# Kernel tuning notes

Measured on AMD Instinct MI355X. Metric: run time of the kernel, lower is better.

Reference implementation:

```python
import jax, jax.numpy as jnp
import numpy as np

B, OUT, IN = 512, 1024, 1024


def setup_inputs() -> dict:
    key = jax.random.key(0)
    k1, k2 = jax.random.split(key)
    X = jax.random.normal(k1, (B, IN), dtype=jnp.float32)
    # xavier_uniform for W: bound = sqrt(6/(in+out))
    bound = float(np.sqrt(6.0 / (IN + OUT)))
    W = jax.random.uniform(k2, (OUT, IN), dtype=jnp.float32, minval=-bound, maxval=bound)
    factors = jnp.ones((OUT, 1), dtype=jnp.float32)
    return {"X": X, "W": W, "factors": factors}


def reference(X, W, factors):
    # tropical (max-plus) matmul with per-output-row scaling of X:
    # out[b,o] = max_i ( W[o,i] + X[b,i] * factors[o] )
    sum_var = W[None, :, :] + X[:, None, :] * factors[None, :, :]  # (B, OUT, IN)
    return jnp.max(sum_var, axis=-1)  # (B, OUT)
```

## Files before the change

### kernel.cpp

```cpp
#include <hip/hip_runtime.h>
#include <stdint.h>


#define BDIM 512
#define OUTDIM 1024
#define INDIM 1024
#define BM 64
#define BN 64
#define BK 32
#define SPLITK 4
#define KCHUNK (INDIM / SPLITK)

__device__ __forceinline__ unsigned enc_f32(float f) {
    unsigned u = __float_as_uint(f);
    return (u & 0x80000000u) ? ~u : (u | 0x80000000u);
}
__device__ __forceinline__ float dec_f32(unsigned k) {
    unsigned u = (k & 0x80000000u) ? (k & 0x7FFFFFFFu) : ~k;
    return __uint_as_float(u);
}

__global__ __launch_bounds__(256, 2)
void smp_main_kernel(const float* __restrict__ X, const float* __restrict__ W,
                     const float* __restrict__ F, unsigned* __restrict__ outk) {
    __shared__ float Xs[BK][BM + 4];
    __shared__ float Ws[BK][BN + 4];
    __shared__ float Os[BM][BN + 1];

    const int tid = threadIdx.x;
    const int tx = tid & 15;
    const int ty = tid >> 4;
    const int ob = blockIdx.x * BN;
    const int bb = blockIdx.y * BM;
    const int kbase = blockIdx.z * KCHUNK;

    float f[4];
#pragma unroll
    for (int n = 0; n < 4; ++n) f[n] = F[ob + 4 * ty + n];

    float acc[4][4];
#pragma unroll
    for (int m = 0; m < 4; ++m)
#pragma unroll
        for (int n = 0; n < 4; ++n) acc[m][n] = -INFINITY;

    for (int kt = 0; kt < KCHUNK; kt += BK) {
#pragma unroll
        for (int r = 0; r < 2; ++r) {
            const int l2 = tid + r * 256;
            const int row = l2 >> 3;
            const int c4 = (l2 & 7) * 4;
            const float4 xv = *reinterpret_cast<const float4*>(
                &X[(size_t)(bb + row) * INDIM + kbase + kt + c4]);
            const float4 wv = *reinterpret_cast<const float4*>(
                &W[(size_t)(ob + row) * INDIM + kbase + kt + c4]);
            Xs[c4 + 0][row] = xv.x; Xs[c4 + 1][row] = xv.y;
            Xs[c4 + 2][row] = xv.z; Xs[c4 + 3][row] = xv.w;
            Ws[c4 + 0][row] = wv.x; Ws[c4 + 1][row] = wv.y;
            Ws[c4 + 2][row] = wv.z; Ws[c4 + 3][row] = wv.w;
        }
        __syncthreads();

#pragma unroll
        for (int i = 0; i < BK; ++i) {
            const float4 xv = *reinterpret_cast<const float4*>(&Xs[i][4 * tx]);
            const float4 wv = *reinterpret_cast<const float4*>(&Ws[i][4 * ty]);
            const float x[4] = {xv.x, xv.y, xv.z, xv.w};
            const float w[4] = {wv.x, wv.y, wv.z, wv.w};
#pragma unroll
            for (int m = 0; m < 4; ++m)
#pragma unroll
                for (int n = 0; n < 4; ++n)
                    acc[m][n] = fmaxf(acc[m][n], fmaf(x[m], f[n], w[n]));
        }
        __syncthreads();
    }

#pragma unroll
    for (int m = 0; m < 4; ++m)
#pragma unroll
        for (int n = 0; n < 4; ++n)
            Os[4 * tx + m][4 * ty + n] = acc[m][n];
    __syncthreads();

#pragma unroll
    for (int c = 0; c < 16; ++c) {
        const int flat = c * 256 + tid;
        const int bl = flat >> 6;
        const int ol = flat & 63;
        const unsigned key = enc_f32(Os[bl][ol]);
        atomicMax(&outk[(size_t)(bb + bl) * OUTDIM + ob + ol], key);
    }
}

__global__ __launch_bounds__(256)
void smp_decode_kernel(unsigned* __restrict__ data) {
    const int idx = blockIdx.x * 256 + threadIdx.x;
    uint4 v = reinterpret_cast<uint4*>(data)[idx];
    float4 o;
    o.x = dec_f32(v.x); o.y = dec_f32(v.y); o.z = dec_f32(v.z); o.w = dec_f32(v.w);
    reinterpret_cast<float4*>(data)[idx] = o;
}

extern "C" void kernel_launch(void* const* d_in, const int* in_sizes, int n_in,
                              void* d_out, int out_size, void* d_ws, size_t ws_size,
                              hipStream_t stream) {
    const float* X = (const float*)d_in[0];
    const float* W = (const float*)d_in[1];
    const float* F = (const float*)d_in[2];
    unsigned* outk = (unsigned*)d_out;

    hipMemsetAsync(d_out, 0, (size_t)out_size * sizeof(float), stream);

    dim3 grid(OUTDIM / BN, BDIM / BM, SPLITK);
    smp_main_kernel<<<grid, 256, 0, stream>>>(X, W, F, outk);

    const int nvec = out_size / 4;
    smp_decode_kernel<<<nvec / 256, 256, 0, stream>>>(outk);
}
```

Before: 96.41 us.

## Use 128x128 register tiles with split-K slices and a max-reduce combine pass

Enlarges the block tile to 128x128 with 8x8 per-thread accumulators and a single 64-wide K chunk per block, stored in swizzled float4 shared memory so there are no transposing scalar stores. The atomicMax on order-preserving integer keys, the memset and the decode pass are replaced by plain writes of 16 partial slices to the workspace, followed by a combine kernel that takes their max. This raises the compute-to-shared-load ratio and removes the atomics. In exchange it writes and reads 32 MB of workspace and uses 64 accumulators per thread, which risks register pressure under launch_bounds(256,2).

```diff
diff --git a/kernel.cpp b/kernel.cpp
--- a/kernel.cpp
+++ b/kernel.cpp
@@ -5,101 +5,96 @@
 #define BDIM 512
 #define OUTDIM 1024
 #define INDIM 1024
-#define BM 64
-#define BN 64
-#define BK 32
-#define SPLITK 4
-#define KCHUNK (INDIM / SPLITK)
-
-__device__ __forceinline__ unsigned enc_f32(float f) {
-    unsigned u = __float_as_uint(f);
-    return (u & 0x80000000u) ? ~u : (u | 0x80000000u);
-}
-__device__ __forceinline__ float dec_f32(unsigned k) {
-    unsigned u = (k & 0x80000000u) ? (k & 0x7FFFFFFFu) : ~k;
-    return __uint_as_float(u);
-}
+#define BM 128
+#define BN 128
+#define BK 64
+#define SPLITK 16
+#define SLICE_F4 (BDIM * OUTDIM / 4)
 
 __global__ __launch_bounds__(256, 2)
 void smp_main_kernel(const float* __restrict__ X, const float* __restrict__ W,
-                     const float* __restrict__ F, unsigned* __restrict__ outk) {
-    __shared__ float Xs[BK][BM + 4];
-    __shared__ float Ws[BK][BN + 4];
-    __shared__ float Os[BM][BN + 1];
+                     const float* __restrict__ F, float* __restrict__ ws) {
+    __shared__ float4 Xs[BM][BK / 4];
+    __shared__ float4 Ws[BN][BK / 4];
 
     const int tid = threadIdx.x;
     const int tx = tid & 15;
     const int ty = tid >> 4;
     const int ob = blockIdx.x * BN;
     const int bb = blockIdx.y * BM;
-    const int kbase = blockIdx.z * KCHUNK;
-
-    float f[4];
-#pragma unroll
-    for (int n = 0; n < 4; ++n) f[n] = F[ob + 4 * ty + n];
-
-    float acc[4][4];
-#pragma unroll
-    for (int m = 0; m < 4; ++m)
-#pragma unroll
-        for (int n = 0; n < 4; ++n) acc[m][n] = -INFINITY;
-
-    for (int kt = 0; kt < KCHUNK; kt += BK) {
-#pragma unroll
-        for (int r = 0; r < 2; ++r) {
-            const int l2 = tid + r * 256;
-            const int row = l2 >> 3;
-            const int c4 = (l2 & 7) * 4;
-            const float4 xv = *reinterpret_cast<const float4*>(
-                &X[(size_t)(bb + row) * INDIM + kbase + kt + c4]);
-            const float4 wv = *reinterpret_cast<const float4*>(
-                &W[(size_t)(ob + row) * INDIM + kbase + kt + c4]);
-            Xs[c4 + 0][row] = xv.x; Xs[c4 + 1][row] = xv.y;
-            Xs[c4 + 2][row] = xv.z; Xs[c4 + 3][row] = xv.w;
-            Ws[c4 + 0][row] = wv.x; Ws[c4 + 1][row] = wv.y;
-            Ws[c4 + 2][row] = wv.z; Ws[c4 + 3][row] = wv.w;
-        }
-        __syncthreads();
+    const int kb = blockIdx.z * BK;
 
 #pragma unroll
-        for (int i = 0; i < BK; ++i) {
-            const float4 xv = *reinterpret_cast<const float4*>(&Xs[i][4 * tx]);
-            const float4 wv = *reinterpret_cast<const float4*>(&Ws[i][4 * ty]);
-            const float x[4] = {xv.x, xv.y, xv.z, xv.w};
-            const float w[4] = {wv.x, wv.y, wv.z, wv.w};
-#pragma unroll
-            for (int m = 0; m < 4; ++m)
-#pragma unroll
-                for (int n = 0; n < 4; ++n)
-                    acc[m][n] = fmaxf(acc[m][n], fmaf(x[m], f[n], w[n]));
-        }
-        __syncthreads();
+    for (int rr = 0; rr < 8; ++rr) {
+        const int idx = tid + 256 * rr;
+        const int row = idx >> 4;
+        const int c = idx & 15;
+        const int cs = c ^ ((row >> 3) & 7);
+        Xs[row][cs] = *reinterpret_cast<const float4*>(
+            &X[(size_t)(bb + row) * INDIM + kb + 4 * c]);
+        Ws[row][cs] = *reinterpret_cast<const float4*>(
+            &W[(size_t)(ob + row) * INDIM + kb + 4 * c]);
     }
 
+    float f[8];
 #pragma unroll
-    for (int m = 0; m < 4; ++m)
+    for (int n = 0; n < 8; ++n) f[n] = F[ob + 8 * ty + n];
+
+    float acc[8][8];
 #pragma unroll
-        for (int n = 0; n < 4; ++n)
-            Os[4 * tx + m][4 * ty + n] = acc[m][n];
+    for (int m = 0; m < 8; ++m)
+#pragma unroll
+        for (int n = 0; n < 8; ++n) acc[m][n] = -INFINITY;
+
     __syncthreads();
 
+    const int sx = tx & 7;
+    const int sy = ty & 7;
+
+    for (int i4 = 0; i4 < BK / 4; ++i4) {
+        float xr[8][4], wr[8][4];
 #pragma unroll
-    for (int c = 0; c < 16; ++c) {
-        const int flat = c * 256 + tid;
-        const int bl = flat >> 6;
-        const int ol = flat & 63;
-        const unsigned key = enc_f32(Os[bl][ol]);
-        atomicMax(&outk[(size_t)(bb + bl) * OUTDIM + ob + ol], key);
+        for (int m = 0; m < 8; ++m) {
+            const float4 v = Xs[8 * tx + m][i4 ^ sx];
+            xr[m][0] = v.x; xr[m][1] = v.y; xr[m][2] = v.z; xr[m][3] = v.w;
+        }
+#pragma unroll
+        for (int n = 0; n < 8; ++n) {
+            const float4 v = Ws[8 * ty + n][i4 ^ sy];
+            wr[n][0] = v.x; wr[n][1] = v.y; wr[n][2] = v.z; wr[n][3] = v.w;
+        }
+#pragma unroll
+        for (int j = 0; j < 4; ++j)
+#pragma unroll
+            for (int m = 0; m < 8; ++m)
+#pragma unroll
+                for (int n = 0; n < 8; ++n)
+                    acc[m][n] = fmaxf(acc[m][n], fmaf(xr[m][j], f[n], wr[n][j]));
+    }
+
+    float* slice = ws + (size_t)blockIdx.z * BDIM * OUTDIM;
+#pragma unroll
+    for (int m = 0; m < 8; ++m) {
+        float4 lo, hi;
+        lo.x = acc[m][0]; lo.y = acc[m][1]; lo.z = acc[m][2]; lo.w = acc[m][3];
+        hi.x = acc[m][4]; hi.y = acc[m][5]; hi.z = acc[m][6]; hi.w = acc[m][7];
+        float* p = &slice[(size_t)(bb + 8 * tx + m) * OUTDIM + ob + 8 * ty];
+        *reinterpret_cast<float4*>(p) = lo;
+        *reinterpret_cast<float4*>(p + 4) = hi;
     }
 }
 
 __global__ __launch_bounds__(256)
-void smp_decode_kernel(unsigned* __restrict__ data) {
+void smp_combine_kernel(const float4* __restrict__ ws, float4* __restrict__ out) {
     const int idx = blockIdx.x * 256 + threadIdx.x;
-    uint4 v = reinterpret_cast<uint4*>(data)[idx];
-    float4 o;
-    o.x = dec_f32(v.x); o.y = dec_f32(v.y); o.z = dec_f32(v.z); o.w = dec_f32(v.w);
-    reinterpret_cast<float4*>(data)[idx] = o;
+    float4 m = ws[idx];
+#pragma unroll
+    for (int s = 1; s < SPLITK; ++s) {
+        const float4 v = ws[idx + (size_t)s * SLICE_F4];
+        m.x = fmaxf(m.x, v.x); m.y = fmaxf(m.y, v.y);
+        m.z = fmaxf(m.z, v.z); m.w = fmaxf(m.w, v.w);
+    }
+    out[idx] = m;
 }
 
 extern "C" void kernel_launch(void* const* d_in, const int* in_sizes, int n_in,
@@ -108,13 +103,10 @@
     const float* X = (const float*)d_in[0];
     const float* W = (const float*)d_in[1];
     const float* F = (const float*)d_in[2];
-    unsigned* outk = (unsigned*)d_out;
-
-    hipMemsetAsync(d_out, 0, (size_t)out_size * sizeof(float), stream);
 
     dim3 grid(OUTDIM / BN, BDIM / BM, SPLITK);
-    smp_main_kernel<<<grid, 256, 0, stream>>>(X, W, F, outk);
+    smp_main_kernel<<<grid, 256, 0, stream>>>(X, W, F, (float*)d_ws);
 
-    const int nvec = out_size / 4;
-    smp_decode_kernel<<<nvec / 256, 256, 0, stream>>>(outk);
+    smp_combine_kernel<<<SLICE_F4 / 256, 256, 0, stream>>>(
+        (const float4*)d_ws, (float4*)d_out);
 }
```

Result: faster. 92.03 us (-4.5%).
